# Performance work log

Hardware: AMD Instinct MI355X
Metric: run time of the kernel (lower is better)

The kernel has to match this reference:

```python
import jax, jax.numpy as jnp
import numpy as np

B, S, V, D, H, E, A, L = 64, 1024, 32000, 1024, 1024, 1024, 1024, 2


def setup_inputs() -> dict:
    key = jax.random.key(0)
    ks = jax.random.split(key, 24)
    s = 0.02
    d = {}
    d["input_step"] = jax.random.randint(ks[0], (B, 1), 0, V)
    d["h0"] = jax.random.normal(ks[1], (L, B, H), jnp.float32)
    d["c0"] = jax.random.normal(ks[2], (L, B, H), jnp.float32)
    d["encoder_outputs"] = jax.random.normal(ks[3], (B, S, E), jnp.float32)
    # embedding table
    d["emb"] = jax.random.normal(ks[4], (V, D), jnp.float32) * s
    # Bahdanau attention: W1 (decoder hidden -> A), W2 (encoder -> A), v (A -> 1)
    d["Wa_h"] = jax.random.normal(ks[5], (A, H), jnp.float32) * s
    d["ba_h"] = jnp.zeros((A,), jnp.float32)
    d["Wa_e"] = jax.random.normal(ks[6], (A, E), jnp.float32) * s
    d["ba_e"] = jnp.zeros((A,), jnp.float32)
    d["va"] = jax.random.normal(ks[7], (A,), jnp.float32) * s
    d["bva"] = jnp.zeros((), jnp.float32)
    # LSTM layer 0: input dim D+E, gates [i,f,g,o] packed as 4H (PyTorch order)
    d["Wih0"] = jax.random.normal(ks[8], (4 * H, D + E), jnp.float32) * s
    d["Whh0"] = jax.random.normal(ks[9], (4 * H, H), jnp.float32) * s
    d["bih0"] = jnp.zeros((4 * H,), jnp.float32)
    d["bhh0"] = jnp.zeros((4 * H,), jnp.float32)
    # LSTM layer 1: input dim H
    d["Wih1"] = jax.random.normal(ks[10], (4 * H, H), jnp.float32) * s
    d["Whh1"] = jax.random.normal(ks[11], (4 * H, H), jnp.float32) * s
    d["bih1"] = jnp.zeros((4 * H,), jnp.float32)
    d["bhh1"] = jnp.zeros((4 * H,), jnp.float32)
    # output projection
    d["Wout"] = jax.random.normal(ks[12], (V, H), jnp.float32) * s
    d["bout"] = jnp.zeros((V,), jnp.float32)
    return d


def _lstm_cell(x, h, c, Wih, Whh, bih, bhh):
    gates = x @ Wih.T + h @ Whh.T + bih + bhh  # [B, 4H]
    i, f, g, o = jnp.split(gates, 4, axis=-1)  # PyTorch gate order i,f,g,o
    c_new = jax.nn.sigmoid(f) * c + jax.nn.sigmoid(i) * jnp.tanh(g)
    h_new = jax.nn.sigmoid(o) * jnp.tanh(c_new)
    return h_new, c_new


def reference(input_step, h0, c0, encoder_outputs, emb, Wa_h, ba_h, Wa_e, ba_e,
              va, bva, Wih0, Whh0, bih0, bhh0, Wih1, Whh1, bih1, bhh1, Wout, bout):
    # embedding lookup: [B,1] -> [B,D]
    embedded = emb[input_step[:, 0]]
    # Bahdanau attention using top decoder layer hidden state h0[-1]
    q = h0[-1] @ Wa_h.T + ba_h                                   # [B,A]
    k = jnp.einsum('bse,ae->bsa', encoder_outputs, Wa_e) + ba_e  # [B,S,A]
    score = jnp.einsum('bsa,a->bs', jnp.tanh(q[:, None, :] + k), va) + bva
    attn_w = jax.nn.softmax(score, axis=1)                       # [B,S]
    context = jnp.einsum('bs,bse->be', attn_w, encoder_outputs)  # [B,E]
    x = jnp.concatenate([embedded, context], axis=-1)            # [B,D+E]
    # 2-layer LSTM, single time step (inference: no inter-layer dropout)
    h1, c1 = _lstm_cell(x, h0[0], c0[0], Wih0, Whh0, bih0, bhh0)
    h2, c2 = _lstm_cell(h1, h0[1], c0[1], Wih1, Whh1, bih1, bhh1)
    logits = h2 @ Wout.T + bout                                  # [B,V]
    h_new = jnp.stack([h1, h2])
    c_new = jnp.stack([c1, c2])
    return logits, h_new, c_new, attn_w
```

## Files before the change

kernel.cpp:

```cpp
#include <hip/hip_runtime.h>


typedef __attribute__((ext_vector_type(8))) __bf16 bf16x8;
typedef __attribute__((ext_vector_type(4))) __bf16 bf16x4v;
typedef __attribute__((ext_vector_type(4))) float f32x4;

#define GLOADLDS(g, l)                                                         \
  __builtin_amdgcn_global_load_lds(                                            \
      (const __attribute__((address_space(1))) unsigned int*)(g),              \
      (__attribute__((address_space(3))) unsigned int*)(l), 16, 0, 0)

__device__ __forceinline__ ushort4 cvt4(f32x4 v) {
  bf16x4v h = {(__bf16)v.x, (__bf16)v.y, (__bf16)v.z, (__bf16)v.w};
  union { bf16x4v h; ushort4 u; } c; c.h = h; return c.u;
}
__device__ __forceinline__ float bf2f(unsigned short u) {
  return __uint_as_float(((unsigned int)u) << 16);
}
__device__ __forceinline__ float sigm(float x) { return 1.0f / (1.0f + __expf(-x)); }
__device__ __forceinline__ float fast_tanh(float x) {
  return 1.0f - 2.0f / (__expf(2.0f * x) + 1.0f);
}

__global__ __launch_bounds__(256) void cvt_bf_k(const float* __restrict__ in,
                                                unsigned short* __restrict__ out, int n8) {
  int i = blockIdx.x * 256 + threadIdx.x;
  if (i >= n8) return;
  const f32x4* p = (const f32x4*)in + 2 * (size_t)i;
  ushort4* o = (ushort4*)out + 2 * (size_t)i;
  f32x4 a = p[0], b = p[1];
  o[0] = cvt4(a);
  o[1] = cvt4(b);
}

__global__ __launch_bounds__(256) void gather_k(const int* __restrict__ step,
                                                const float* __restrict__ emb,
                                                float* __restrict__ x) {
  int b = blockIdx.x, t = threadIdx.x;
  int row = step[b];
  f32x4 v = *(const f32x4*)(emb + (size_t)row * 1024 + t * 4);
  *(f32x4*)(x + (size_t)b * 2048 + t * 4) = v;
}

__global__ __launch_bounds__(256) void small_gemm(
    const float* __restrict__ A0, int lda0,
    const float* __restrict__ A1, int lda1, int kSplitA,
    const float* __restrict__ B0, int ldb0,
    const float* __restrict__ B1, int ldb1, int kSplitB,
    float* __restrict__ part, int N, int kChunk) {
  __shared__ unsigned short As[64 * 32];
  __shared__ unsigned short Bs[256 * 32];
  int tid = threadIdx.x;
  int n0 = blockIdx.x * 256;
  int k0 = blockIdx.y * kChunk;
  int wave = tid >> 6, lane = tid & 63, quad = lane >> 4, l15 = lane & 15;
  f32x4 acc[4][4] = {};
  for (int kb = k0; kb < k0 + kChunk; kb += 32) {
    const float* Ap; int ldA, kA;
    if (kb < kSplitA) { Ap = A0; ldA = lda0; kA = kb; }
    else              { Ap = A1; ldA = lda1; kA = kb - kSplitA; }
    const float* Bp; int ldB, kB;
    if (kb < kSplitB) { Bp = B0; ldB = ldb0; kB = kb; }
    else              { Bp = B1; ldB = ldb1; kB = kb - kSplitB; }
#pragma unroll
    for (int c = 0; c < 2; c++) {
      int f = c * 256 + tid;
      int row = f >> 3, colf = f & 7;
      f32x4 v = *(const f32x4*)(Ap + (size_t)row * ldA + kA + colf * 4);
      *(ushort4*)&As[row * 32 + colf * 4] = cvt4(v);
    }
#pragma unroll
    for (int c = 0; c < 8; c++) {
      int f = c * 256 + tid;
      int row = f >> 3, colf = f & 7;
      f32x4 v = *(const f32x4*)(Bp + (size_t)(n0 + row) * ldB + kB + colf * 4);
      *(ushort4*)&Bs[row * 32 + colf * 4] = cvt4(v);
    }
    __syncthreads();
    bf16x8 af[4], bfv[4];
#pragma unroll
    for (int rt = 0; rt < 4; rt++)
      af[rt] = *(const bf16x8*)&As[(16 * rt + l15) * 32 + quad * 8];
#pragma unroll
    for (int ct = 0; ct < 4; ct++)
      bfv[ct] = *(const bf16x8*)&Bs[(64 * wave + 16 * ct + l15) * 32 + quad * 8];
#pragma unroll
    for (int rt = 0; rt < 4; rt++)
#pragma unroll
      for (int ct = 0; ct < 4; ct++)
        acc[rt][ct] = __builtin_amdgcn_mfma_f32_16x16x32_bf16(af[rt], bfv[ct], acc[rt][ct], 0, 0, 0);
    __syncthreads();
  }
  size_t base = (size_t)blockIdx.y * 64 * (size_t)N;
#pragma unroll
  for (int rt = 0; rt < 4; rt++)
#pragma unroll
    for (int ct = 0; ct < 4; ct++)
#pragma unroll
      for (int r = 0; r < 4; r++) {
        int m = 16 * rt + 4 * quad + r;
        int n = n0 + 64 * wave + 16 * ct + l15;
        part[base + (size_t)m * N + n] = acc[rt][ct][r];
      }
}

__global__ __launch_bounds__(256) void q_reduce(const float* __restrict__ qpart,
                                                const float* __restrict__ ba_h,
                                                float* __restrict__ q) {
  int idx = blockIdx.x * 256 + threadIdx.x;
  int a = idx & 1023;
  float s = ba_h[a];
#pragma unroll
  for (int sp = 0; sp < 8; sp++) s += qpart[sp * 65536 + idx];
  q[idx] = s;
}


#define SCHED0() __builtin_amdgcn_sched_barrier(0)

#define STAGE_TILE(t)                                                        \
  {                                                                          \
    int _buf = (t) & 1;                                                      \
    const unsigned short* _as = encb + aSrc + (size_t)(t) * 64;              \
    const unsigned short* _bs = Waeb + bSrc + (size_t)(t) * 64;              \
    unsigned short* _la = &sh[_buf * 32768 + wave * 512];                    \
    unsigned short* _lb = &sh[_buf * 32768 + 16384 + wave * 512];            \
    GLOADLDS(_as,          _la);                                             \
    GLOADLDS(_as + 65536,  _la + 4096);                                      \
    GLOADLDS(_as + 131072, _la + 8192);                                      \
    GLOADLDS(_as + 196608, _la + 12288);                                     \
    GLOADLDS(_bs,          _lb);                                             \
    GLOADLDS(_bs + 65536,  _lb + 4096);                                      \
    GLOADLDS(_bs + 131072, _lb + 8192);                                      \
    GLOADLDS(_bs + 196608, _lb + 12288);                                     \
  }

#define LOAD_A(buf, mh)                                                      \
  {                                                                          \
    const unsigned short* _p = &sh[(buf) * 32768 + aRow + (mh) * 4096];      \
    _Pragma("unroll") for (int mr = 0; mr < 4; mr++) {                       \
      a[mr][0] = *(const bf16x8*)&_p[mr * 1024 + cs0];                       \
      a[mr][1] = *(const bf16x8*)&_p[mr * 1024 + cs1];                       \
    }                                                                        \
  }

#define LOAD_B(buf, nh, Bd)                                                  \
  {                                                                          \
    const unsigned short* _p = &sh[(buf) * 32768 + 16384 + bRow + (nh) * 2048]; \
    _Pragma("unroll") for (int nc = 0; nc < 2; nc++) {                       \
      Bd[nc][0] = *(const bf16x8*)&_p[nc * 1024 + cs0];                      \
      Bd[nc][1] = *(const bf16x8*)&_p[nc * 1024 + cs1];                      \
    }                                                                        \
  }

#define MMQ(mh, nh, Bd)                                                      \
  _Pragma("unroll") for (int mr = 0; mr < 4; mr++)                           \
  _Pragma("unroll") for (int nc = 0; nc < 2; nc++)                           \
  _Pragma("unroll") for (int ks = 0; ks < 2; ks++)                           \
    acc[(mh) * 4 + mr][(nh) * 2 + nc] = __builtin_amdgcn_mfma_f32_16x16x32_bf16( \
        a[mr][ks], Bd[nc][ks], acc[(mh) * 4 + mr][(nh) * 2 + nc], 0, 0, 0);

#define PH_WAIT_LGKM()                                                       \
  SCHED0();                                                                  \
  __builtin_amdgcn_s_barrier();                                              \
  asm volatile("s_waitcnt lgkmcnt(0)" ::: "memory");                         \
  SCHED0();

#define PH_END()                                                             \
  SCHED0();                                                                  \
  __builtin_amdgcn_s_barrier();                                              \
  SCHED0();

#define GROUP(c, MODE)                                                       \
  {                                                                          \
    int buf = (c) & 1;                                                       \
                    \
    LOAD_A(buf, 0);                                                          \
    LOAD_B(buf, 0, b0);                                                      \
    PH_WAIT_LGKM();                                                          \
    __builtin_amdgcn_s_setprio(1); MMQ(0, 0, b0); __builtin_amdgcn_s_setprio(0); \
    PH_END();                                                                \
                                      \
    LOAD_B(buf, 1, b1);                                                      \
    PH_WAIT_LGKM();                                                          \
    __builtin_amdgcn_s_setprio(1); MMQ(0, 1, b1); __builtin_amdgcn_s_setprio(0); \
    PH_END();                                                                \
                                      \
    LOAD_A(buf, 1);                                                          \
    PH_WAIT_LGKM();                                                          \
    __builtin_amdgcn_s_setprio(1); MMQ(1, 0, b0); __builtin_amdgcn_s_setprio(0); \
    PH_END();                                                                \
     \
    if ((MODE) == 0) { STAGE_TILE((c) + 2); }                                \
    if ((MODE) == 0) asm volatile("s_waitcnt vmcnt(8)" ::: "memory");        \
    if ((MODE) == 1) asm volatile("s_waitcnt vmcnt(0)" ::: "memory");        \
    SCHED0();                                                                \
    __builtin_amdgcn_s_barrier();                                            \
    SCHED0();                                                                \
    __builtin_amdgcn_s_setprio(1); MMQ(1, 1, b1); __builtin_amdgcn_s_setprio(0); \
    PH_END();                                                                \
  }

__global__ __launch_bounds__(512, 2) void attn_gemm_8p(
    const unsigned short* __restrict__ encb, const unsigned short* __restrict__ Waeb,
    const float* __restrict__ q, const float* __restrict__ ba_e,
    const float* __restrict__ va, float* __restrict__ score) {
  __shared__ unsigned short sh[65536];
  __shared__ float red[256];
  int tid = threadIdx.x;
  int wave = tid >> 6, lane = tid & 63, quad = lane >> 4, l15 = lane & 15;
  int wr = wave >> 2, wc = wave & 3;

  int h = blockIdx.y * 4 + blockIdx.x;
  int lgc = (h & 7) * 128 + (h >> 3);
  int m0 = (lgc >> 2) * 256, n0 = (lgc & 3) * 256;

  int srow = wave * 8 + (lane >> 3);
  int sslot = ((lane & 7) ^ (lane >> 3)) * 8;
  size_t aSrc = (size_t)(m0 + srow) * 1024 + sslot;
  size_t bSrc = (size_t)(n0 + srow) * 1024 + sslot;

  int aRow = (wr * 128 + l15) * 64;
  int bRow = (wc * 64 + l15) * 64;
  int cs0 = (quad ^ (l15 & 7)) * 8;
  int cs1 = ((4 + quad) ^ (l15 & 7)) * 8;

  bf16x8 a[4][2], b0[2][2], b1[2][2];
  f32x4 acc[8][4] = {};

  STAGE_TILE(0);
  STAGE_TILE(1);
  asm volatile("s_waitcnt vmcnt(8)" ::: "memory");
  SCHED0();
  __builtin_amdgcn_s_barrier();
  SCHED0();

  for (int c = 0; c < 14; ++c) GROUP(c, 0);
  GROUP(14, 1);
  GROUP(15, 2);

  __syncthreads();
  if (tid < 256) red[tid] = 0.0f;
  __syncthreads();
  int b = m0 >> 10;
  float qe[4], vv[4];
#pragma unroll
  for (int j = 0; j < 4; j++) {
    int n = n0 + wc * 64 + j * 16 + l15;
    qe[j] = q[b * 1024 + n] + ba_e[n];
    vv[j] = va[n];
  }
#pragma unroll
  for (int i = 0; i < 8; i++)
#pragma unroll
    for (int r = 0; r < 4; r++) {
      float p = 0.0f;
#pragma unroll
      for (int j = 0; j < 4; j++)
        p += vv[j] * fast_tanh(qe[j] + acc[i][j][r]);
      p += __shfl_xor(p, 1); p += __shfl_xor(p, 2);
      p += __shfl_xor(p, 4); p += __shfl_xor(p, 8);
      if (l15 == 0) atomicAdd(&red[wr * 128 + i * 16 + quad * 4 + r], p);
    }
  __syncthreads();
  if (tid < 256) atomicAdd(&score[m0 + tid], red[tid]);
}

#undef GROUP
#undef PH_END
#undef PH_WAIT_LGKM
#undef MMQ
#undef LOAD_B
#undef LOAD_A
#undef STAGE_TILE
#undef SCHED0

__global__ __launch_bounds__(512) void attn_gemm_f32(
    const float* __restrict__ enc, const float* __restrict__ Wae,
    const float* __restrict__ q, const float* __restrict__ ba_e,
    const float* __restrict__ va, float* __restrict__ score) {
  __shared__ unsigned short As[128 * 32];
  __shared__ unsigned short Bs[256 * 32];
  __shared__ float red[128];
  int tid = threadIdx.x;
  int n0 = blockIdx.x * 256, m0 = blockIdx.y * 128;
  int wave = tid >> 6, lane = tid & 63, quad = lane >> 4, l15 = lane & 15;
  int wr = wave >> 2, wc = wave & 3;
  f32x4 acc[4][4] = {};
  for (int kb = 0; kb < 1024; kb += 32) {
#pragma unroll
    for (int c = 0; c < 2; c++) {
      int f = c * 512 + tid;
      int row = f >> 3, colf = f & 7;
      f32x4 v = *(const f32x4*)(enc + (size_t)(m0 + row) * 1024 + kb + colf * 4);
      *(ushort4*)&As[row * 32 + colf * 4] = cvt4(v);
    }
#pragma unroll
    for (int c = 0; c < 4; c++) {
      int f = c * 512 + tid;
      int row = f >> 3, colf = f & 7;
      f32x4 v = *(const f32x4*)(Wae + (size_t)(n0 + row) * 1024 + kb + colf * 4);
      *(ushort4*)&Bs[row * 32 + colf * 4] = cvt4(v);
    }
    __syncthreads();
    bf16x8 af[4], bfv[4];
#pragma unroll
    for (int rt = 0; rt < 4; rt++)
      af[rt] = *(const bf16x8*)&As[(64 * wr + 16 * rt + l15) * 32 + quad * 8];
#pragma unroll
    for (int ct = 0; ct < 4; ct++)
      bfv[ct] = *(const bf16x8*)&Bs[(64 * wc + 16 * ct + l15) * 32 + quad * 8];
#pragma unroll
    for (int rt = 0; rt < 4; rt++)
#pragma unroll
      for (int ct = 0; ct < 4; ct++)
        acc[rt][ct] = __builtin_amdgcn_mfma_f32_16x16x32_bf16(af[rt], bfv[ct], acc[rt][ct], 0, 0, 0);
    __syncthreads();
  }
  int b = m0 >> 10;
  if (tid < 128) red[tid] = 0.0f;
  __syncthreads();
  float qe[4], vv[4];
#pragma unroll
  for (int ct = 0; ct < 4; ct++) {
    int n = n0 + 64 * wc + 16 * ct + l15;
    qe[ct] = q[b * 1024 + n] + ba_e[n];
    vv[ct] = va[n];
  }
#pragma unroll
  for (int rt = 0; rt < 4; rt++)
#pragma unroll
    for (int r = 0; r < 4; r++) {
      float p = 0.0f;
#pragma unroll
      for (int ct = 0; ct < 4; ct++)
        p += vv[ct] * tanhf(qe[ct] + acc[rt][ct][r]);
      p += __shfl_xor(p, 1); p += __shfl_xor(p, 2);
      p += __shfl_xor(p, 4); p += __shfl_xor(p, 8);
      if (l15 == 0) atomicAdd(&red[64 * wr + 16 * rt + 4 * quad + r], p);
    }
  __syncthreads();
  if (tid < 128) atomicAdd(&score[m0 + tid], red[tid]);
}

__global__ __launch_bounds__(256) void softmax_k(const float* __restrict__ score,
                                                 float* __restrict__ attnw) {
  int b = blockIdx.x, tid = threadIdx.x;
  __shared__ float wred[4];
  float v[4];
  float mx = -1e30f;
#pragma unroll
  for (int i = 0; i < 4; i++) {
    v[i] = score[b * 1024 + tid + 256 * i];
    mx = fmaxf(mx, v[i]);
  }
  for (int off = 1; off < 64; off <<= 1) mx = fmaxf(mx, __shfl_xor(mx, off));
  int w = tid >> 6;
  if ((tid & 63) == 0) wred[w] = mx;
  __syncthreads();
  mx = fmaxf(fmaxf(wred[0], wred[1]), fmaxf(wred[2], wred[3]));
  float s = 0.0f;
#pragma unroll
  for (int i = 0; i < 4; i++) { v[i] = __expf(v[i] - mx); s += v[i]; }
  for (int off = 1; off < 64; off <<= 1) s += __shfl_xor(s, off);
  __syncthreads();
  if ((tid & 63) == 0) wred[w] = s;
  __syncthreads();
  s = wred[0] + wred[1] + wred[2] + wred[3];
  float inv = 1.0f / s;
#pragma unroll
  for (int i = 0; i < 4; i++) attnw[b * 1024 + tid + 256 * i] = v[i] * inv;
}

__global__ __launch_bounds__(256) void context_bf(const unsigned short* __restrict__ encb,
                                                  const float* __restrict__ attnw,
                                                  float* __restrict__ ctxpart) {
  int b = blockIdx.x, sc = blockIdx.y, tid = threadIdx.x;
  __shared__ float w[128];
  if (tid < 128) w[tid] = attnw[b * 1024 + sc * 128 + tid];
  __syncthreads();
  const unsigned short* ep = encb + (size_t)b * 1048576 + (size_t)sc * 128 * 1024 + tid * 4;
  f32x4 a0 = {}, a1 = {};
  for (int s = 0; s < 128; s += 2) {
    ushort4 u0 = *(const ushort4*)(ep + (size_t)s * 1024);
    ushort4 u1 = *(const ushort4*)(ep + (size_t)(s + 1) * 1024);
    float w0 = w[s], w1 = w[s + 1];
    a0.x += w0 * bf2f(u0.x); a0.y += w0 * bf2f(u0.y);
    a0.z += w0 * bf2f(u0.z); a0.w += w0 * bf2f(u0.w);
    a1.x += w1 * bf2f(u1.x); a1.y += w1 * bf2f(u1.y);
    a1.z += w1 * bf2f(u1.z); a1.w += w1 * bf2f(u1.w);
  }
  f32x4 r = a0 + a1;
  *(f32x4*)(ctxpart + ((size_t)sc * 64 + b) * 1024 + tid * 4) = r;
}

__global__ __launch_bounds__(256) void ctx_reduce(const float* __restrict__ ctxpart,
                                                  float* __restrict__ x) {
  int idx = blockIdx.x * 256 + threadIdx.x;
  int b = idx >> 10, e = idx & 1023;
  float s = 0.0f;
#pragma unroll
  for (int sc = 0; sc < 8; sc++) s += ctxpart[((size_t)sc * 64 + b) * 1024 + e];
  x[(size_t)b * 2048 + 1024 + e] = s;
}

__global__ __launch_bounds__(256) void context_k(const float* __restrict__ enc,
                                                 const float* __restrict__ attnw,
                                                 float* __restrict__ x) {
  __shared__ float w[1024];
  int b = blockIdx.y, e0 = blockIdx.x * 256, tid = threadIdx.x;
#pragma unroll
  for (int i = 0; i < 4; i++) w[tid + 256 * i] = attnw[b * 1024 + tid + 256 * i];
  __syncthreads();
  const float* ep = enc + (size_t)b * 1024 * 1024 + e0 + tid;
  float acc = 0.0f;
#pragma unroll 4
  for (int s = 0; s < 1024; s++) acc += w[s] * ep[(size_t)s * 1024];
  x[(size_t)b * 2048 + 1024 + e0 + tid] = acc;
}

__global__ __launch_bounds__(256) void cell_k(const float* __restrict__ part, int nsplit,
                                              const float* __restrict__ bih,
                                              const float* __restrict__ bhh,
                                              const float* __restrict__ cin,
                                              float* __restrict__ hout,
                                              float* __restrict__ cout) {
  int idx = blockIdx.x * 256 + threadIdx.x;
  int b = idx >> 10, h = idx & 1023;
  float gi = bih[h] + bhh[h];
  float gf = bih[1024 + h] + bhh[1024 + h];
  float gg = bih[2048 + h] + bhh[2048 + h];
  float go = bih[3072 + h] + bhh[3072 + h];
  const float* p = part + (size_t)b * 4096 + h;
  for (int sp = 0; sp < nsplit; sp++, p += 262144) {
    gi += p[0]; gf += p[1024]; gg += p[2048]; go += p[3072];
  }
  float c = sigm(gf) * cin[idx] + sigm(gi) * tanhf(gg);
  float hh = sigm(go) * tanhf(c);
  cout[idx] = c;
  hout[idx] = hh;
}

__global__ __launch_bounds__(256) void logits_reduce(const float* __restrict__ part,
                                                     const float* __restrict__ bout,
                                                     float* __restrict__ out) {
  int v = blockIdx.x * 256 + threadIdx.x;
  int b = blockIdx.y;
  size_t i = (size_t)b * 32000 + v;
  out[i] = bout[v] + part[i] + part[2048000 + i];
}

extern "C" void kernel_launch(void* const* d_in, const int* in_sizes, int n_in,
                              void* d_out, int out_size, void* d_ws, size_t ws_size,
                              hipStream_t stream) {
  const int*   input_step = (const int*)d_in[0];
  const float* h0   = (const float*)d_in[1];
  const float* c0   = (const float*)d_in[2];
  const float* enc  = (const float*)d_in[3];
  const float* emb  = (const float*)d_in[4];
  const float* Wa_h = (const float*)d_in[5];
  const float* ba_h = (const float*)d_in[6];
  const float* Wa_e = (const float*)d_in[7];
  const float* ba_e = (const float*)d_in[8];
  const float* va   = (const float*)d_in[9];
  const float* Wih0 = (const float*)d_in[11];
  const float* Whh0 = (const float*)d_in[12];
  const float* bih0 = (const float*)d_in[13];
  const float* bhh0 = (const float*)d_in[14];
  const float* Wih1 = (const float*)d_in[15];
  const float* Whh1 = (const float*)d_in[16];
  const float* bih1 = (const float*)d_in[17];
  const float* bhh1 = (const float*)d_in[18];
  const float* Wout = (const float*)d_in[19];
  const float* bout = (const float*)d_in[20];

  float* out    = (float*)d_out;
  float* logits = out;
  float* h1o    = out + 2048000;
  float* h2o    = out + 2113536;
  float* c1o    = out + 2179072;
  float* c2o    = out + 2244608;
  float* attnw  = out + 2310144;

  float* ws      = (float*)d_ws;
  float* x       = ws;
  float* q       = ws + 131072;
  float* score   = ws + 196608;
  float* part    = ws + 262144;
  float* ctxpart = ws + 4358144;
  unsigned short* Waeb = (unsigned short*)(ws + 4882432);
  unsigned short* encb = (unsigned short*)(ws + 6979584);
  const bool big = ws_size >= 162136064ull;

  gather_k<<<64, 256, 0, stream>>>(input_step, emb, x);

  small_gemm<<<dim3(4, 8), 256, 0, stream>>>(
      h0 + 65536, 1024, h0 + 65536, 1024, 1024,
      Wa_h, 1024, Wa_h, 1024, 1024,
      part, 1024, 128);
  q_reduce<<<256, 256, 0, stream>>>(part, ba_h, q);

  hipMemsetAsync(score, 0, 65536 * sizeof(float), stream);

  if (big) {
    cvt_bf_k<<<512, 256, 0, stream>>>(Wa_e, Waeb, 131072);
    cvt_bf_k<<<32768, 256, 0, stream>>>(enc, encb, 8388608);
    attn_gemm_8p<<<dim3(4, 256), 512, 0, stream>>>(encb, Waeb, q, ba_e, va, score);
    softmax_k<<<64, 256, 0, stream>>>(score, attnw);
    context_bf<<<dim3(64, 8), 256, 0, stream>>>(encb, attnw, ctxpart);
    ctx_reduce<<<256, 256, 0, stream>>>(ctxpart, x);
  } else {
    attn_gemm_f32<<<dim3(4, 512), 512, 0, stream>>>(enc, Wa_e, q, ba_e, va, score);
    softmax_k<<<64, 256, 0, stream>>>(score, attnw);
    context_k<<<dim3(4, 64), 256, 0, stream>>>(enc, attnw, x);
  }

  small_gemm<<<dim3(16, 12), 256, 0, stream>>>(
      x, 2048, h0, 1024, 2048,
      Wih0, 2048, Whh0, 1024, 2048,
      part, 4096, 256);
  cell_k<<<256, 256, 0, stream>>>(part, 12, bih0, bhh0, c0, h1o, c1o);

  small_gemm<<<dim3(16, 8), 256, 0, stream>>>(
      h1o, 1024, h0 + 65536, 1024, 1024,
      Wih1, 1024, Whh1, 1024, 1024,
      part, 4096, 256);
  cell_k<<<256, 256, 0, stream>>>(part, 8, bih1, bhh1, c0 + 65536, h2o, c2o);

  small_gemm<<<dim3(125, 2), 256, 0, stream>>>(
      h2o, 1024, h2o, 1024, 1024,
      Wout, 1024, Wout, 1024, 1024,
      part, 32000, 512);
  logits_reduce<<<dim3(125, 64), 256, 0, stream>>>(part, bout, logits);
}
```

Measured before the change: 867.3 us.

## Interleave next-tile LDS staging across MFMA phases with one barrier per phase

Restructures the attention GEMM main loop. The old loop prefetched two tiles ahead, issued each tile's whole load in one burst and used two barriers per phase. The new loop prefetches one tile ahead and splits the global-to-LDS loads into four two-load chunks, one per MFMA phase, with a single barrier per phase and finer vmcnt waits. The goal is to spread memory traffic over the compute, cut barrier count and keep the loop rolled. The cost is a shorter prefetch distance, so global latency is less hidden, and the double-buffer reuse now depends on careful barrier and waitcnt ordering.

After: 854.9 us. No clear change (-1.4%).

```diff
diff --git a/kernel.cpp b/kernel.cpp
--- a/kernel.cpp
+++ b/kernel.cpp
@@ -117,22 +117,21 @@
 
 
 #define SCHED0() __builtin_amdgcn_sched_barrier(0)
-
-#define STAGE_TILE(t)                                                        \
+#define VMCNT(n) asm volatile("s_waitcnt vmcnt(" #n ")" ::: "memory")
+
+#define STAGE_A2(bufv, t, j0v, j1v)                                          \
   {                                                                          \
-    int _buf = (t) & 1;                                                      \
-    const unsigned short* _as = encb + aSrc + (size_t)(t) * 64;              \
-    const unsigned short* _bs = Waeb + bSrc + (size_t)(t) * 64;              \
-    unsigned short* _la = &sh[_buf * 32768 + wave * 512];                    \
-    unsigned short* _lb = &sh[_buf * 32768 + 16384 + wave * 512];            \
-    GLOADLDS(_as,          _la);                                             \
-    GLOADLDS(_as + 65536,  _la + 4096);                                      \
-    GLOADLDS(_as + 131072, _la + 8192);                                      \
-    GLOADLDS(_as + 196608, _la + 12288);                                     \
-    GLOADLDS(_bs,          _lb);                                             \
-    GLOADLDS(_bs + 65536,  _lb + 4096);                                      \
-    GLOADLDS(_bs + 131072, _lb + 8192);                                      \
-    GLOADLDS(_bs + 196608, _lb + 12288);                                     \
+    const unsigned short* _s = encb + aSrc + (size_t)(t) * 64;               \
+    unsigned short* _l = &sh[(bufv) * 32768 + wave * 512];                   \
+    GLOADLDS(_s + (j0v) * 65536, _l + (j0v) * 4096);                         \
+    GLOADLDS(_s + (j1v) * 65536, _l + (j1v) * 4096);                         \
+  }
+#define STAGE_B2(bufv, t, j0v, j1v)                                          \
+  {                                                                          \
+    const unsigned short* _s = Waeb + bSrc + (size_t)(t) * 64;               \
+    unsigned short* _l = &sh[(bufv) * 32768 + 16384 + wave * 512];           \
+    GLOADLDS(_s + (j0v) * 65536, _l + (j0v) * 4096);                         \
+    GLOADLDS(_s + (j1v) * 65536, _l + (j1v) * 4096);                         \
   }
 
 #define LOAD_A(buf, mh)                                                      \
@@ -160,45 +159,59 @@
     acc[(mh) * 4 + mr][(nh) * 2 + nc] = __builtin_amdgcn_mfma_f32_16x16x32_bf16( \
         a[mr][ks], Bd[nc][ks], acc[(mh) * 4 + mr][(nh) * 2 + nc], 0, 0, 0);
 
-#define PH_WAIT_LGKM()                                                       \
+#define PHASE_SYNC()                                                         \
   SCHED0();                                                                  \
   __builtin_amdgcn_s_barrier();                                              \
   asm volatile("s_waitcnt lgkmcnt(0)" ::: "memory");                         \
   SCHED0();
 
-#define PH_END()                                                             \
-  SCHED0();                                                                  \
-  __builtin_amdgcn_s_barrier();                                              \
+#define P_MFMA(mh, nh, Bd)                                                   \
+  __builtin_amdgcn_s_setprio(1); MMQ(mh, nh, Bd); __builtin_amdgcn_s_setprio(0); \
   SCHED0();
 
-#define GROUP(c, MODE)                                                       \
+#define GROUP_MAIN(c)                                                        \
+  {                                                                          \
+    int buf = (c) & 1, nbuf = buf ^ 1;                                       \
+                                                                     \
+    STAGE_A2(nbuf, (c) + 1, 0, 2);                                           \
+    LOAD_A(buf, 0);                                                          \
+    LOAD_B(buf, 0, b0);                                                      \
+    PHASE_SYNC();                                                            \
+    P_MFMA(0, 0, b0);                                                        \
+                                                                     \
+    STAGE_B2(nbuf, (c) + 1, 0, 1);                                           \
+    LOAD_B(buf, 1, b1);                                                      \
+    VMCNT(4);                        \
+    PHASE_SYNC();                                                            \
+    P_MFMA(0, 1, b1);                                                        \
+                                                                     \
+    STAGE_B2(nbuf, (c) + 1, 2, 3);                                           \
+    LOAD_A(buf, 1);                                                          \
+    PHASE_SYNC();                                                            \
+    P_MFMA(1, 0, b0);                                                        \
+                                                                     \
+    STAGE_A2(nbuf, (c) + 1, 1, 3);                                           \
+    VMCNT(2);              \
+    PHASE_SYNC();                                                            \
+    P_MFMA(1, 1, b1);                                                        \
+  }
+
+#define GROUP_TAIL(c)                                                        \
   {                                                                          \
     int buf = (c) & 1;                                                       \
-                    \
     LOAD_A(buf, 0);                                                          \
     LOAD_B(buf, 0, b0);                                                      \
-    PH_WAIT_LGKM();                                                          \
-    __builtin_amdgcn_s_setprio(1); MMQ(0, 0, b0); __builtin_amdgcn_s_setprio(0); \
-    PH_END();                                                                \
-                                      \
+    PHASE_SYNC();                                                            \
+    P_MFMA(0, 0, b0);                                                        \
     LOAD_B(buf, 1, b1);                                                      \
-    PH_WAIT_LGKM();                                                          \
-    __builtin_amdgcn_s_setprio(1); MMQ(0, 1, b1); __builtin_amdgcn_s_setprio(0); \
-    PH_END();                                                                \
-                                      \
+    VMCNT(0);                       \
+    PHASE_SYNC();                                                            \
+    P_MFMA(0, 1, b1);                                                        \
     LOAD_A(buf, 1);                                                          \
-    PH_WAIT_LGKM();                                                          \
-    __builtin_amdgcn_s_setprio(1); MMQ(1, 0, b0); __builtin_amdgcn_s_setprio(0); \
-    PH_END();                                                                \
-     \
-    if ((MODE) == 0) { STAGE_TILE((c) + 2); }                                \
-    if ((MODE) == 0) asm volatile("s_waitcnt vmcnt(8)" ::: "memory");        \
-    if ((MODE) == 1) asm volatile("s_waitcnt vmcnt(0)" ::: "memory");        \
-    SCHED0();                                                                \
-    __builtin_amdgcn_s_barrier();                                            \
-    SCHED0();                                                                \
-    __builtin_amdgcn_s_setprio(1); MMQ(1, 1, b1); __builtin_amdgcn_s_setprio(0); \
-    PH_END();                                                                \
+    PHASE_SYNC();                                                            \
+    P_MFMA(1, 0, b0);                                                        \
+    PHASE_SYNC();                                                            \
+    P_MFMA(1, 1, b1);                                                        \
   }
 
 __global__ __launch_bounds__(512, 2) void attn_gemm_8p(
@@ -228,16 +241,18 @@
   bf16x8 a[4][2], b0[2][2], b1[2][2];
   f32x4 acc[8][4] = {};
 
-  STAGE_TILE(0);
-  STAGE_TILE(1);
-  asm volatile("s_waitcnt vmcnt(8)" ::: "memory");
+  STAGE_A2(0, 0, 0, 2);
+  STAGE_B2(0, 0, 0, 1);
+  STAGE_B2(0, 0, 2, 3);
+  STAGE_A2(0, 0, 1, 3);
+  VMCNT(2);
   SCHED0();
   __builtin_amdgcn_s_barrier();
   SCHED0();
 
-  for (int c = 0; c < 14; ++c) GROUP(c, 0);
-  GROUP(14, 1);
-  GROUP(15, 2);
+#pragma unroll 1
+  for (int c = 0; c < 15; ++c) GROUP_MAIN(c);
+  GROUP_TAIL(15);
 
   __syncthreads();
   if (tid < 256) red[tid] = 0.0f;
@@ -266,13 +281,16 @@
   if (tid < 256) atomicAdd(&score[m0 + tid], red[tid]);
 }
 
-#undef GROUP
-#undef PH_END
-#undef PH_WAIT_LGKM
+#undef GROUP_TAIL
+#undef GROUP_MAIN
+#undef P_MFMA
+#undef PHASE_SYNC
 #undef MMQ
 #undef LOAD_B
 #undef LOAD_A
-#undef STAGE_TILE
+#undef STAGE_B2
+#undef STAGE_A2
+#undef VMCNT
 #undef SCHED0
 
 __global__ __launch_bounds__(512) void attn_gemm_f32(
```
